# Kernel optimization log

Hardware: AMD Instinct MI355X
Metric: run time of the kernel (lower is better)

The kernel has to match this reference:

```python
import jax, jax.numpy as jnp
import numpy as np

B, T, IN, H, OUT = 64, 1024, 64, 512, 64


def setup_inputs() -> dict:
    key = jax.random.key(0)
    ks = jax.random.split(key, 11)
    s = 0.05  # small init to avoid gate saturation
    return {
        "x": jax.random.normal(ks[0], (B, T, IN), jnp.float32),
        "W_ih1": jax.random.normal(ks[1], (4 * H, IN), jnp.float32) * s,
        "W_hh1": jax.random.normal(ks[2], (4 * H, H), jnp.float32) * s,
        "b_ih1": jax.random.normal(ks[3], (4 * H,), jnp.float32) * s,
        "b_hh1": jax.random.normal(ks[4], (4 * H,), jnp.float32) * s,
        "W_ih2": jax.random.normal(ks[5], (4 * H, H), jnp.float32) * s,
        "W_hh2": jax.random.normal(ks[6], (4 * H, H), jnp.float32) * s,
        "b_ih2": jax.random.normal(ks[7], (4 * H,), jnp.float32) * s,
        "b_hh2": jax.random.normal(ks[8], (4 * H,), jnp.float32) * s,
        "W_out": jax.random.normal(ks[9], (OUT, H), jnp.float32) * s,
        "b_out": jax.random.normal(ks[10], (OUT,), jnp.float32) * s,
    }


def _lstm_cell(x_t, h, c, W_ih, W_hh, b_ih, b_hh):
    # PyTorch LSTMCell: gates ordered i, f, g, o
    gates = x_t @ W_ih.T + b_ih + h @ W_hh.T + b_hh  # [B, 4H]
    i, f, g, o = jnp.split(gates, 4, axis=-1)
    i = jax.nn.sigmoid(i)
    f = jax.nn.sigmoid(f)
    g = jnp.tanh(g)
    o = jax.nn.sigmoid(o)
    c_new = f * c + i * g
    h_new = o * jnp.tanh(c_new)
    return h_new, c_new


def reference(x, W_ih1, W_hh1, b_ih1, b_hh1, W_ih2, W_hh2, b_ih2, b_hh2,
              W_out, b_out):
    batch = x.shape[0]
    h1 = jnp.zeros((batch, W_hh1.shape[1]), x.dtype)
    c1 = jnp.zeros_like(h1)
    h2 = jnp.zeros((batch, W_hh2.shape[1]), x.dtype)
    c2 = jnp.zeros_like(h2)

    def step(carry, x_t):
        h1, c1, h2, c2 = carry
        h1, c1 = _lstm_cell(x_t, h1, c1, W_ih1, W_hh1, b_ih1, b_hh1)
        h2, c2 = _lstm_cell(h1, h2, c2, W_ih2, W_hh2, b_ih2, b_hh2)
        y_t = h2 @ W_out.T + b_out  # per-step Linear head
        return (h1, c1, h2, c2), y_t

    xs = jnp.swapaxes(x, 0, 1)  # [T, B, IN]
    _, ys = jax.lax.scan(step, (h1, c1, h2, c2), xs)
    return jnp.swapaxes(ys, 0, 1)  # [B, T, OUT]
```

## Files before the change

kernel.cpp:

```cpp
#include <hip/hip_runtime.h>

#define B_    64
#define T_    1024
#define IN_   64
#define H_    512
#define OUT_  64
#define SLOTS 8
#define NWG   130
#define NWORD 6144

typedef _Float16 f16;
typedef _Float16 half8 __attribute__((ext_vector_type(8)));
typedef float    floatx4 __attribute__((ext_vector_type(4)));
typedef unsigned int u32;
typedef unsigned short u16;
typedef unsigned long long u64;

#define MFMA16(a,b,c) __builtin_amdgcn_mfma_f32_16x16x32_f16((a),(b),(c),0,0,0)

#define XS_OFF   0
#define HB_OFF   8192
#define CC_OFF   9216
#define RED_OFF  11264
#define H1W_OFF  44032
#define H2W_OFF  101376

__device__ __forceinline__ float sigmoidf_(float x) {
    return 1.0f / (1.0f + __expf(-x));
}
__device__ __forceinline__ float tanhf_(float x) {
    float ax = fabsf(x);
    float e  = __expf(-2.0f * ax);
    float t  = (1.0f - e) / (1.0f + e);
    return x >= 0.0f ? t : -t;
}

__device__ __forceinline__ void wait_ge(u32* p, u32 v) {
    while (__hip_atomic_load(p, __ATOMIC_RELAXED, __HIP_MEMORY_SCOPE_AGENT) < v)
        __builtin_amdgcn_s_sleep(1);
}
__device__ __forceinline__ void flag_add(u32* p) {
    __hip_atomic_fetch_add(p, 1u, __ATOMIC_RELAXED, __HIP_MEMORY_SCOPE_AGENT);
}
__device__ __forceinline__ void astore8w(u64* p, u64 v) {
    __hip_atomic_store(p, v, __ATOMIC_RELAXED, __HIP_MEMORY_SCOPE_SYSTEM);
}
__device__ __forceinline__ u64 aload8w(const u64* p) {
    return __hip_atomic_load(p, __ATOMIC_RELAXED, __HIP_MEMORY_SCOPE_SYSTEM);
}

__device__ __forceinline__ void stage_poll(char* smem, int ldsOff, const u64* g,
                                           u32 exp, int tid, const int* soff) {
    u32 pend = 0xFFFu;
    do {
        u64 vv[12];
        #pragma unroll
        for (int i = 0; i < 12; ++i)
            vv[i] = aload8w(g + i*512 + tid);
        #pragma unroll
        for (int i = 0; i < 12; ++i) {
            if ((pend & (1u << i)) && (u32)(vv[i] >> 48) == exp) {
                *(u64*)(smem + ldsOff + soff[i]) = vv[i];
                pend &= ~(1u << i);
            }
        }
        if (pend) __builtin_amdgcn_s_sleep(1);
    } while (pend);
}

__device__ __forceinline__ half8 frag_pk(const char* p) {
    const u64* q = (const u64*)p;
    u64 w0 = q[0], w1 = q[1], w2 = q[2];
    u32 b = (u32)(w0 >> 32), c = (u32)w1, d = (u32)(w1 >> 32);
    union { u32 u[4]; half8 h; } U;
    U.u[0] = (u32)w0;
    U.u[1] = (b & 0xffffu) | (c << 16);
    U.u[2] = (c >> 16) | (d << 16);
    U.u[3] = (u32)w2;
    return U.h;
}
#define WB(jt,row,wi) (((jt)*224 + (row)*7 + (wi)) * 8)

__global__ void pack_w1(const float* __restrict__ Wih, const float* __restrict__ Whh,
                        f16* __restrict__ Wp) {
    int idx = blockIdx.x * 256 + threadIdx.x;
    if (idx >= 4*32*18*512) return;
    int j    = idx & 7;
    int lane = (idx >> 3) & 63;
    int kt   = (idx >> 9) % 18;
    int r    = (idx >> 9) / 18;
    int jt   = r & 31;
    int g    = r >> 5;
    int n = g*512 + jt*16 + (lane & 15);
    int k = kt*32 + (lane >> 4)*8 + j;
    float v = (k < 64) ? Wih[n*64 + k] : Whh[n*512 + (k - 64)];
    Wp[idx] = (f16)v;
}

__global__ void pack_w2(const float* __restrict__ Wih, const float* __restrict__ Whh,
                        f16* __restrict__ Wp) {
    int idx = blockIdx.x * 256 + threadIdx.x;
    if (idx >= 4*32*32*512) return;
    int j    = idx & 7;
    int lane = (idx >> 3) & 63;
    int kt   = (idx >> 9) & 31;
    int r    = idx >> 14;
    int jt   = r & 31;
    int g    = r >> 5;
    int n = g*512 + jt*16 + (lane & 15);
    int k = kt*32 + (lane >> 4)*8 + j;
    float v = (k < 512) ? Wih[n*512 + k] : Whh[n*512 + (k - 512)];
    Wp[idx] = (f16)v;
}

__global__ void pack_wo(const float* __restrict__ Wout, f16* __restrict__ Wp) {
    int idx = blockIdx.x * 256 + threadIdx.x;
    if (idx >= 4*16*512) return;
    int j    = idx & 7;
    int lane = (idx >> 3) & 63;
    int kt   = (idx >> 9) & 15;
    int nt   = idx >> 13;
    int n = nt*16 + (lane & 15);
    int k = kt*32 + (lane >> 4)*8 + j;
    Wp[idx] = (f16)Wout[n*512 + k];
}

__global__ void bias_sum(const float* __restrict__ a1, const float* __restrict__ b1,
                         const float* __restrict__ a2, const float* __restrict__ b2,
                         float* __restrict__ s1, float* __restrict__ s2) {
    int i = blockIdx.x * 256 + threadIdx.x;
    if (i >= 2048) return;
    s1[i] = a1[i] + b1[i];
    s2[i] = a2[i] + b2[i];
}

__global__ __launch_bounds__(512, 1) void lstm_persist(
    const float* __restrict__ x,
    const f16*  __restrict__ W1p,
    const f16*  __restrict__ W2p,
    const f16*  __restrict__ Wop,
    const float* __restrict__ bs1,
    const float* __restrict__ bs2,
    const float* __restrict__ bout,
    u64*  __restrict__ h1w,
    u64*  __restrict__ h2w,
    float* __restrict__ y,
    u32*  __restrict__ arr2,
    u32*  __restrict__ arrH)
{
    __shared__ __align__(16) char smem[158720];
    float* RED = (float*)(smem + RED_OFF);
    float* CC  = (float*)(smem + CC_OFF);

    const int wg   = blockIdx.x;
    const int tid  = threadIdx.x;
    const int lane = tid & 63;
    const int w    = tid >> 6;
    const int col  = lane & 15;
    const int quad = lane >> 4;

    int soff[12];
    #pragma unroll
    for (int i = 0; i < 12; ++i) {
        const int ww = i*512 + tid;
        const int jt_ = ww / 192, rr = ww - jt_*192;
        soff[i] = WB(jt_, rr/6, rr%6);
    }
    const int pr  = tid / 6, pi = tid - pr*6;
    const int pj  = pi % 3;
    const int pc0 = pr*16 + (pi/3)*8 + pj*3;
    const u16* hb = (const u16*)(smem + HB_OFF);

    if (wg < 64) {
        const int jt = wg & 31, bhalf = wg >> 5;
        const int gp = w & 1, kq = w >> 1;
        half8 wrx[2];
        half8 wrh[2][4];
        if (kq < 2) {
            #pragma unroll
            for (int gi = 0; gi < 2; ++gi)
                wrx[gi] = *(const half8*)(W1p + ((size_t)(((gp*2+gi)*32 + jt)*18 + kq)*64 + lane)*8);
        }
        #pragma unroll
        for (int gi = 0; gi < 2; ++gi)
            #pragma unroll
            for (int k = 0; k < 4; ++k) {
                const int kt = 2 + kq*4 + k;
                wrh[gi][k] = *(const half8*)(W1p + ((size_t)(((gp*2+gi)*32 + jt)*18 + kt)*64 + lane)*8);
            }
        float bsr[4];
        #pragma unroll
        for (int g = 0; g < 4; ++g) bsr[g] = bs1[g*512 + jt*16 + (tid & 15)];
        CC[tid] = 0.f;

        u32* a2 = arr2 + bhalf*1024;

        {
            const int lb = tid >> 4, kc4 = tid & 15;
            const float* src = x + ((size_t)(bhalf*32 + lb)*T_ + 0)*(size_t)IN_ + ((kc4 ^ (lb & 7)) * 4);
            *(float4*)(smem + XS_OFF + tid*16) = *(const float4*)src;
        }
        stage_poll(smem, H1W_OFF, h1w + (size_t)(7*2 + bhalf)*NWORD, 0u, tid, soff);
        __syncthreads();

        for (int t = 0; t < T_; ++t) {
            floatx4 acc[2][2] = {{{0.f,0.f,0.f,0.f},{0.f,0.f,0.f,0.f}},
                                 {{0.f,0.f,0.f,0.f},{0.f,0.f,0.f,0.f}}};
            #pragma unroll
            for (int m = 0; m < 2; ++m) {
                const int lb_a = m*16 + col, sw = lb_a & 7;
                if (kq < 2) {
                    const int fg = kq*8 + quad*2;
                    float4 u = *(const float4*)(smem + XS_OFF + ((size_t)lb_a*16 + (fg ^ sw))*16);
                    float4 v = *(const float4*)(smem + XS_OFF + ((size_t)lb_a*16 + ((fg+1) ^ sw))*16);
                    half8 a = (half8){(f16)u.x,(f16)u.y,(f16)u.z,(f16)u.w,
                                      (f16)v.x,(f16)v.y,(f16)v.z,(f16)v.w};
                    acc[0][m] = MFMA16(a, wrx[0], acc[0][m]);
                    acc[1][m] = MFMA16(a, wrx[1], acc[1][m]);
                }
                #pragma unroll
                for (int k = 0; k < 4; ++k) {
                    const int kc = kq*16 + k*4 + quad;
                    half8 a = frag_pk(smem + H1W_OFF + WB(kc>>1, lb_a, (kc&1)*3));
                    acc[0][m] = MFMA16(a, wrh[0][k], acc[0][m]);
                    acc[1][m] = MFMA16(a, wrh[1][k], acc[1][m]);
                }
            }
            #pragma unroll
            for (int gi = 0; gi < 2; ++gi) {
                const int g = gp*2 + gi;
                #pragma unroll
                for (int m = 0; m < 2; ++m)
                    #pragma unroll
                    for (int r = 0; r < 4; ++r)
                        RED[kq*2048 + g*512 + (m*16 + quad*4 + r)*16 + col] = acc[gi][m][r];
            }
            __syncthreads();
            {
                float gt[4];
                #pragma unroll
                for (int g = 0; g < 4; ++g)
                    gt[g] = RED[       g*512 + tid] + RED[2048 + g*512 + tid]
                          + RED[4096 + g*512 + tid] + RED[6144 + g*512 + tid] + bsr[g];
                const float i_ = sigmoidf_(gt[0]);
                const float f_ = sigmoidf_(gt[1]);
                const float g_ = tanhf_(gt[2]);
                const float o_ = sigmoidf_(gt[3]);
                const float cn = f_ * CC[tid] + i_ * g_;
                CC[tid] = cn;
                ((f16*)(smem + HB_OFF))[tid] = (f16)(o_ * tanhf_(cn));
            }
            __syncthreads();
            if (tid < 192) {
                u64 wv = (u64)hb[pc0] | ((u64)hb[pc0+1] << 16)
                       | ((pj < 2) ? ((u64)hb[pc0+2] << 32) : 0)
                       | ((u64)(u32)(t + 1) << 48);
                astore8w(h1w + (size_t)((t & 7)*2 + bhalf)*NWORD + jt*192 + tid, wv);
            }
            if (tid == 0 && t + 1 < T_ && t + 1 >= SLOTS)
                wait_ge(a2 + (t + 1 - SLOTS), 32u);
            if (t + 1 < T_) {
                {
                    const int lb = tid >> 4, kc4 = tid & 15;
                    const float* src = x + ((size_t)(bhalf*32 + lb)*T_ + (t+1))*(size_t)IN_ + ((kc4 ^ (lb & 7)) * 4);
                    *(float4*)(smem + XS_OFF + tid*16) = *(const float4*)src;
                }
                stage_poll(smem, H1W_OFF, h1w + (size_t)((t & 7)*2 + bhalf)*NWORD,
                           (u32)(t + 1), tid, soff);
            }
            __syncthreads();
        }
    } else if (wg < 128) {
        const int v = wg - 64;
        const int jt = v & 31, bhalf = v >> 5;
        const int gp = w & 1, kq = w >> 1;
        half8 wrA[2][4], wrB[2][4];
        #pragma unroll
        for (int gi = 0; gi < 2; ++gi)
            #pragma unroll
            for (int k = 0; k < 4; ++k) {
                const int ktA = kq*4 + k;
                const int ktB = 16 + kq*4 + k;
                wrA[gi][k] = *(const half8*)(W2p + ((size_t)(((gp*2+gi)*32 + jt)*32 + ktA)*64 + lane)*8);
                wrB[gi][k] = *(const half8*)(W2p + ((size_t)(((gp*2+gi)*32 + jt)*32 + ktB)*64 + lane)*8);
            }
        float bsr[4];
        #pragma unroll
        for (int g = 0; g < 4; ++g) bsr[g] = bs2[g*512 + jt*16 + (tid & 15)];
        CC[tid] = 0.f;

        u32* a2 = arr2 + bhalf*1024;
        u32* aH = arrH + bhalf*1024;

        stage_poll(smem, H1W_OFF, h1w + (size_t)(0*2 + bhalf)*NWORD, 1u, tid, soff);
        stage_poll(smem, H2W_OFF, h2w + (size_t)(7*2 + bhalf)*NWORD, 0u, tid, soff);
        __syncthreads();

        for (int t2 = 0; t2 < T_; ++t2) {
            floatx4 acc[2][2] = {{{0.f,0.f,0.f,0.f},{0.f,0.f,0.f,0.f}},
                                 {{0.f,0.f,0.f,0.f},{0.f,0.f,0.f,0.f}}};
            #pragma unroll
            for (int m = 0; m < 2; ++m) {
                const int lb_a = m*16 + col;
                #pragma unroll
                for (int k = 0; k < 4; ++k) {
                    const int kc = kq*16 + k*4 + quad;
                    half8 a = frag_pk(smem + H1W_OFF + WB(kc>>1, lb_a, (kc&1)*3));
                    acc[0][m] = MFMA16(a, wrA[0][k], acc[0][m]);
                    acc[1][m] = MFMA16(a, wrA[1][k], acc[1][m]);
                }
            }
            #pragma unroll
            for (int m = 0; m < 2; ++m) {
                const int lb_a = m*16 + col;
                #pragma unroll
                for (int k = 0; k < 4; ++k) {
                    const int kc = kq*16 + k*4 + quad;
                    half8 a = frag_pk(smem + H2W_OFF + WB(kc>>1, lb_a, (kc&1)*3));
                    acc[0][m] = MFMA16(a, wrB[0][k], acc[0][m]);
                    acc[1][m] = MFMA16(a, wrB[1][k], acc[1][m]);
                }
            }
            #pragma unroll
            for (int gi = 0; gi < 2; ++gi) {
                const int g = gp*2 + gi;
                #pragma unroll
                for (int m = 0; m < 2; ++m)
                    #pragma unroll
                    for (int r = 0; r < 4; ++r)
                        RED[kq*2048 + g*512 + (m*16 + quad*4 + r)*16 + col] = acc[gi][m][r];
            }
            __syncthreads();
            {
                float gt[4];
                #pragma unroll
                for (int g = 0; g < 4; ++g)
                    gt[g] = RED[       g*512 + tid] + RED[2048 + g*512 + tid]
                          + RED[4096 + g*512 + tid] + RED[6144 + g*512 + tid] + bsr[g];
                const float i_ = sigmoidf_(gt[0]);
                const float f_ = sigmoidf_(gt[1]);
                const float g_ = tanhf_(gt[2]);
                const float o_ = sigmoidf_(gt[3]);
                const float cn = f_ * CC[tid] + i_ * g_;
                CC[tid] = cn;
                ((f16*)(smem + HB_OFF))[tid] = (f16)(o_ * tanhf_(cn));
            }
            __syncthreads();
            if (tid < 192) {
                u64 wv = (u64)hb[pc0] | ((u64)hb[pc0+1] << 16)
                       | ((pj < 2) ? ((u64)hb[pc0+2] << 32) : 0)
                       | ((u64)(u32)(t2 + 1) << 48);
                astore8w(h2w + (size_t)((t2 & 7)*2 + bhalf)*NWORD + jt*192 + tid, wv);
            }
            if (tid == 0) flag_add(a2 + t2);
            if (tid == 0 && t2 + 1 < T_ && t2 + 1 >= SLOTS)
                wait_ge(aH + (t2 + 1 - SLOTS), 1u);
            if (t2 + 1 < T_) {
                stage_poll(smem, H1W_OFF, h1w + (size_t)(((t2+1) & 7)*2 + bhalf)*NWORD,
                           (u32)(t2 + 2), tid, soff);
                stage_poll(smem, H2W_OFF, h2w + (size_t)((t2 & 7)*2 + bhalf)*NWORD,
                           (u32)(t2 + 1), tid, soff);
            }
            __syncthreads();
        }
    } else {
        const int bhalf = wg - 128;
        const int nt = w & 3, kh = w >> 2;
        half8 wr[8];
        #pragma unroll
        for (int k = 0; k < 8; ++k) {
            const int kt = kh*8 + k;
            wr[k] = *(const half8*)(Wop + ((size_t)(nt*16 + kt)*64 + lane)*8);
        }
        const float boutr = bout[nt*16 + col];
        u32* aH = arrH + bhalf*1024;
        const int lb0 = col, lb1 = 16 + col;

        stage_poll(smem, H1W_OFF, h2w + (size_t)(0*2 + bhalf)*NWORD, 1u, tid, soff);
        __syncthreads();
        if (tid == 0) flag_add(aH + 0);

        for (int t3 = 0; t3 < T_; ++t3) {
            floatx4 acc0 = {0.f,0.f,0.f,0.f}, acc1 = {0.f,0.f,0.f,0.f};
            #pragma unroll
            for (int k = 0; k < 8; ++k) {
                const int kc = (kh*8 + k)*4 + quad;
                half8 a0  = frag_pk(smem + H1W_OFF + WB(kc>>1, lb0, (kc&1)*3));
                half8 a1v = frag_pk(smem + H1W_OFF + WB(kc>>1, lb1, (kc&1)*3));
                acc0 = MFMA16(a0,  wr[k], acc0);
                acc1 = MFMA16(a1v, wr[k], acc1);
            }
            if (kh == 1) {
                #pragma unroll
                for (int r = 0; r < 4; ++r) {
                    RED[(nt*2+0)*256 + (quad*4 + r)*16 + col] = acc0[r];
                    RED[(nt*2+1)*256 + (quad*4 + r)*16 + col] = acc1[r];
                }
            }
            __syncthreads();
            if (kh == 0) {
                #pragma unroll
                for (int r = 0; r < 4; ++r) {
                    const float v0 = acc0[r] + RED[(nt*2+0)*256 + (quad*4 + r)*16 + col] + boutr;
                    const float v1 = acc1[r] + RED[(nt*2+1)*256 + (quad*4 + r)*16 + col] + boutr;
                    const int b0 = bhalf*32 +  0 + quad*4 + r;
                    const int b1 = bhalf*32 + 16 + quad*4 + r;
                    y[((size_t)b0*T_ + t3)*OUT_ + nt*16 + col] = v0;
                    y[((size_t)b1*T_ + t3)*OUT_ + nt*16 + col] = v1;
                }
            }
            __syncthreads();
            if (t3 + 1 < T_) {
                stage_poll(smem, H1W_OFF, h2w + (size_t)(((t3+1) & 7)*2 + bhalf)*NWORD,
                           (u32)(t3 + 2), tid, soff);
                __syncthreads();
                if (tid == 0) flag_add(aH + (t3 + 1));
            }
        }
    }
}

extern "C" void kernel_launch(void* const* d_in, const int* in_sizes, int n_in,
                              void* d_out, int out_size, void* d_ws, size_t ws_size,
                              hipStream_t stream) {
    const float* x    = (const float*)d_in[0];
    const float* Wih1 = (const float*)d_in[1];
    const float* Whh1 = (const float*)d_in[2];
    const float* bih1 = (const float*)d_in[3];
    const float* bhh1 = (const float*)d_in[4];
    const float* Wih2 = (const float*)d_in[5];
    const float* Whh2 = (const float*)d_in[6];
    const float* bih2 = (const float*)d_in[7];
    const float* bhh2 = (const float*)d_in[8];
    const float* Wout = (const float*)d_in[9];
    const float* bout = (const float*)d_in[10];
    float* y = (float*)d_out;

    char* ws = (char*)d_ws;
    f16*   W1p   = (f16*)(ws + 0);
    f16*   W2p   = (f16*)(ws + 2359296);
    f16*   Wop   = (f16*)(ws + 6553600);
    float* bs1   = (float*)(ws + 6619136);
    float* bs2   = (float*)(ws + 6627328);
    u64*   h1w   = (u64*)(ws + 6635520);
    u64*   h2w   = (u64*)(ws + 7421952);
    u32*   arr2  = (u32*)(ws + 8208384);
    u32*   arrH  = (u32*)(ws + 8216576);

    hipMemsetAsync(ws + 6635520, 0, 1589248, stream);

    pack_w1<<<4608, 256, 0, stream>>>(Wih1, Whh1, W1p);
    pack_w2<<<8192, 256, 0, stream>>>(Wih2, Whh2, W2p);
    pack_wo<<<128, 256, 0, stream>>>(Wout, Wop);
    bias_sum<<<8, 256, 0, stream>>>(bih1, bhh1, bih2, bhh2, bs1, bs2);

    lstm_persist<<<NWG, 512, 0, stream>>>(x, W1p, W2p, Wop, bs1, bs2, bout,
                                          h1w, h2w, y, arr2, arrH);
}
```

Before: 4.754 ms.

## Publish hidden state via wave shuffles, merge polls, cache flag waits

Keeps the cell state in registers instead of LDS and publishes the packed fp16 hidden words directly from each wave using lane shuffles. This removes the per-step LDS round trip and one block-wide barrier. The layer-2 blocks now poll the h1 and h2 exchange buffers together in a single loop instead of two sequential loops, overlapping their latency. Slot-reuse waits probe a few steps ahead and cache the result, so most steps skip the global flag spin. The risk is more shuffle and atomic-load traffic per step, plus subtle ordering between the packed words and the rows each wave owns.

```diff
diff --git a/kernel.cpp b/kernel.cpp
--- a/kernel.cpp
+++ b/kernel.cpp
@@ -19,8 +19,6 @@
 #define MFMA16(a,b,c) __builtin_amdgcn_mfma_f32_16x16x32_f16((a),(b),(c),0,0,0)
 
 #define XS_OFF   0
-#define HB_OFF   8192
-#define CC_OFF   9216
 #define RED_OFF  11264
 #define H1W_OFF  44032
 #define H2W_OFF  101376
@@ -42,6 +40,15 @@
 __device__ __forceinline__ void flag_add(u32* p) {
     __hip_atomic_fetch_add(p, 1u, __ATOMIC_RELAXED, __HIP_MEMORY_SCOPE_AGENT);
 }
+__device__ __forceinline__ void cached_wait(u32* arr, int need, u32 thr, int* cache) {
+    if (need <= *cache) return;
+    int probe = need + 4; if (probe > T_ - 1) probe = T_ - 1;
+    if (__hip_atomic_load(arr + probe, __ATOMIC_RELAXED, __HIP_MEMORY_SCOPE_AGENT) >= thr) {
+        *cache = probe; return;
+    }
+    wait_ge(arr + need, thr);
+    *cache = need;
+}
 __device__ __forceinline__ void astore8w(u64* p, u64 v) {
     __hip_atomic_store(p, v, __ATOMIC_RELAXED, __HIP_MEMORY_SCOPE_SYSTEM);
 }
@@ -66,6 +73,32 @@
         }
         if (pend) __builtin_amdgcn_s_sleep(1);
     } while (pend);
+}
+
+__device__ __forceinline__ void stage_poll2(char* smem, const u64* g1, u32 e1,
+                                            const u64* g2, u32 e2,
+                                            int tid, const int* soff) {
+    u32 p1 = 0xFFFu, p2 = 0xFFFu;
+    do {
+        u64 v1[12], v2[12];
+        #pragma unroll
+        for (int i = 0; i < 12; ++i) {
+            v2[i] = aload8w(g2 + i*512 + tid);
+            v1[i] = aload8w(g1 + i*512 + tid);
+        }
+        #pragma unroll
+        for (int i = 0; i < 12; ++i) {
+            if ((p2 & (1u << i)) && (u32)(v2[i] >> 48) == e2) {
+                *(u64*)(smem + H2W_OFF + soff[i]) = v2[i];
+                p2 &= ~(1u << i);
+            }
+            if ((p1 & (1u << i)) && (u32)(v1[i] >> 48) == e1) {
+                *(u64*)(smem + H1W_OFF + soff[i]) = v1[i];
+                p1 &= ~(1u << i);
+            }
+        }
+        if (p1 | p2) __builtin_amdgcn_s_sleep(1);
+    } while (p1 | p2);
 }
 
 __device__ __forceinline__ half8 frag_pk(const char* p) {
@@ -80,6 +113,30 @@
     return U.h;
 }
 #define WB(jt,row,wi) (((jt)*224 + (row)*7 + (wi)) * 8)
+
+__device__ __forceinline__ void shuf_publish(u64* dst, int tid, int tag, float hf) {
+    union { f16 h; u16 u; } cv; cv.h = (f16)hf;
+    int hv = cv.u;
+    const int l  = tid & 63;
+    const int wv = tid >> 6;
+    const int rj = l / 6;
+    const int pi = l - rj*6;
+    const int pj = pi % 3;
+    const int pcb = (pi/3)*8 + pj*3;
+    const int s0 = (rj*16 + pcb)     & 63;
+    const int s1 = (rj*16 + pcb + 1) & 63;
+    const int s2 = (rj*16 + pcb + 2) & 63;
+    int v0 = __shfl(hv, s0, 64);
+    int v1 = __shfl(hv, s1, 64);
+    int v2 = __shfl(hv, s2, 64);
+    if (l < 24) {
+        u64 wvd = (u64)(u16)v0 | ((u64)(u16)v1 << 16)
+                | ((pj < 2) ? ((u64)(u16)v2 << 32) : 0)
+                | ((u64)(u32)tag << 48);
+        const int row = wv*4 + rj;
+        astore8w(dst + row*6 + pi, wvd);
+    }
+}
 
 __global__ void pack_w1(const float* __restrict__ Wih, const float* __restrict__ Whh,
                         f16* __restrict__ Wp) {
@@ -150,7 +207,6 @@
 {
     __shared__ __align__(16) char smem[158720];
     float* RED = (float*)(smem + RED_OFF);
-    float* CC  = (float*)(smem + CC_OFF);
 
     const int wg   = blockIdx.x;
     const int tid  = threadIdx.x;
@@ -166,10 +222,6 @@
         const int jt_ = ww / 192, rr = ww - jt_*192;
         soff[i] = WB(jt_, rr/6, rr%6);
     }
-    const int pr  = tid / 6, pi = tid - pr*6;
-    const int pj  = pi % 3;
-    const int pc0 = pr*16 + (pi/3)*8 + pj*3;
-    const u16* hb = (const u16*)(smem + HB_OFF);
 
     if (wg < 64) {
         const int jt = wg & 31, bhalf = wg >> 5;
@@ -191,7 +243,8 @@
         float bsr[4];
         #pragma unroll
         for (int g = 0; g < 4; ++g) bsr[g] = bs1[g*512 + jt*16 + (tid & 15)];
-        CC[tid] = 0.f;
+        float creg = 0.f;
+        int okA2 = -1;
 
         u32* a2 = arr2 + bhalf*1024;
 
@@ -246,19 +299,13 @@
                 const float f_ = sigmoidf_(gt[1]);
                 const float g_ = tanhf_(gt[2]);
                 const float o_ = sigmoidf_(gt[3]);
-                const float cn = f_ * CC[tid] + i_ * g_;
-                CC[tid] = cn;
-                ((f16*)(smem + HB_OFF))[tid] = (f16)(o_ * tanhf_(cn));
-            }
-            __syncthreads();
-            if (tid < 192) {
-                u64 wv = (u64)hb[pc0] | ((u64)hb[pc0+1] << 16)
-                       | ((pj < 2) ? ((u64)hb[pc0+2] << 32) : 0)
-                       | ((u64)(u32)(t + 1) << 48);
-                astore8w(h1w + (size_t)((t & 7)*2 + bhalf)*NWORD + jt*192 + tid, wv);
+                const float cn = f_ * creg + i_ * g_;
+                creg = cn;
+                shuf_publish(h1w + (size_t)((t & 7)*2 + bhalf)*NWORD + jt*192,
+                             tid, t + 1, o_ * tanhf_(cn));
             }
             if (tid == 0 && t + 1 < T_ && t + 1 >= SLOTS)
-                wait_ge(a2 + (t + 1 - SLOTS), 32u);
+                cached_wait(a2, t + 1 - SLOTS, 32u, &okA2);
             if (t + 1 < T_) {
                 {
                     const int lb = tid >> 4, kc4 = tid & 15;
@@ -287,13 +334,14 @@
         float bsr[4];
         #pragma unroll
         for (int g = 0; g < 4; ++g) bsr[g] = bs2[g*512 + jt*16 + (tid & 15)];
-        CC[tid] = 0.f;
+        float creg = 0.f;
+        int okAH = -1;
 
         u32* a2 = arr2 + bhalf*1024;
         u32* aH = arrH + bhalf*1024;
 
-        stage_poll(smem, H1W_OFF, h1w + (size_t)(0*2 + bhalf)*NWORD, 1u, tid, soff);
-        stage_poll(smem, H2W_OFF, h2w + (size_t)(7*2 + bhalf)*NWORD, 0u, tid, soff);
+        stage_poll2(smem, h1w + (size_t)(0*2 + bhalf)*NWORD, 1u,
+                          h2w + (size_t)(7*2 + bhalf)*NWORD, 0u, tid, soff);
         __syncthreads();
 
         for (int t2 = 0; t2 < T_; ++t2) {
@@ -341,25 +389,18 @@
                 const float f_ = sigmoidf_(gt[1]);
                 const float g_ = tanhf_(gt[2]);
                 const float o_ = sigmoidf_(gt[3]);
-                const float cn = f_ * CC[tid] + i_ * g_;
-                CC[tid] = cn;
-                ((f16*)(smem + HB_OFF))[tid] = (f16)(o_ * tanhf_(cn));
-            }
-            __syncthreads();
-            if (tid < 192) {
-                u64 wv = (u64)hb[pc0] | ((u64)hb[pc0+1] << 16)
-                       | ((pj < 2) ? ((u64)hb[pc0+2] << 32) : 0)
-                       | ((u64)(u32)(t2 + 1) << 48);
-                astore8w(h2w + (size_t)((t2 & 7)*2 + bhalf)*NWORD + jt*192 + tid, wv);
+                const float cn = f_ * creg + i_ * g_;
+                creg = cn;
+                shuf_publish(h2w + (size_t)((t2 & 7)*2 + bhalf)*NWORD + jt*192,
+                             tid, t2 + 1, o_ * tanhf_(cn));
             }
             if (tid == 0) flag_add(a2 + t2);
             if (tid == 0 && t2 + 1 < T_ && t2 + 1 >= SLOTS)
-                wait_ge(aH + (t2 + 1 - SLOTS), 1u);
+                cached_wait(aH, t2 + 1 - SLOTS, 1u, &okAH);
             if (t2 + 1 < T_) {
-                stage_poll(smem, H1W_OFF, h1w + (size_t)(((t2+1) & 7)*2 + bhalf)*NWORD,
-                           (u32)(t2 + 2), tid, soff);
-                stage_poll(smem, H2W_OFF, h2w + (size_t)((t2 & 7)*2 + bhalf)*NWORD,
-                           (u32)(t2 + 1), tid, soff);
+                stage_poll2(smem, h1w + (size_t)(((t2+1) & 7)*2 + bhalf)*NWORD, (u32)(t2 + 2),
+                                  h2w + (size_t)((t2 & 7)*2 + bhalf)*NWORD,     (u32)(t2 + 1),
+                            tid, soff);
             }
             __syncthreads();
         }
```

Measured after the change: 7.107 ms. +49.5%, slower.
